# Kernel optimization log

Measured on AMD Instinct MI355X. Metric: run time of the kernel, lower is better.

Reference implementation:

```python
import jax, jax.numpy as jnp
import numpy as np

V = 163842  # ico6 sphere vertex count
C_IN = 64
C_OUT = 64


def setup_inputs() -> dict:
    key = jax.random.key(0)
    k1, k2, k3, k4 = jax.random.split(key, 4)
    x = jax.random.normal(k1, (2, V, C_IN), dtype=jnp.float32)
    neigh_orders = jax.random.randint(k2, (V * 7,), 0, V, dtype=jnp.int64)
    W = jax.random.normal(k3, (C_OUT, 7 * C_IN), dtype=jnp.float32) * 0.05
    b = jax.random.normal(k4, (C_OUT,), dtype=jnp.float32) * 0.05
    return {"x": x, "neigh_orders": neigh_orders, "W": W, "b": b}


def reference(x, neigh_orders, W, b):
    B, Vn, C = x.shape
    # gather 7 neighbors per vertex: (B, V*7, C) -> (B, V, 7*C)
    mat = x[:, neigh_orders].reshape(B, Vn, 7 * C)
    # Linear: mat @ W.T + b -> (B, V, C_out)
    return jnp.einsum('bvk,ok->bvo', mat, W) + b
```

## Files before the change

kernel.cpp:

```cpp
#include <hip/hip_runtime.h>


constexpr int V_ICO   = 163842;
constexpr int M_TOTAL = 2 * V_ICO;
constexpr int X_ELEMS = M_TOTAL * 64;
constexpr int W_ELEMS = 64 * 448;
constexpr int XCH     = X_ELEMS / 8;
constexpr int WCH     = W_ELEMS / 8;

typedef __attribute__((ext_vector_type(4))) float          f32x4;
typedef __attribute__((ext_vector_type(4))) unsigned int   u32x4;
typedef __attribute__((ext_vector_type(8))) unsigned short u16x8;
typedef __attribute__((ext_vector_type(8))) __bf16         bf16x8;

union BF8 { u32x4 q; u16x8 u; bf16x8 v; };

static __device__ __forceinline__ unsigned short f2bf(float f) {
  unsigned int t = __float_as_uint(f);
  t += 0x7FFFu + ((t >> 16) & 1u);
  return (unsigned short)(t >> 16);
}

static __device__ __forceinline__ u32x4 cvt8(f32x4 a, f32x4 b) {
  BF8 r;
  r.u[0] = f2bf(a[0]); r.u[1] = f2bf(a[1]); r.u[2] = f2bf(a[2]); r.u[3] = f2bf(a[3]);
  r.u[4] = f2bf(b[0]); r.u[5] = f2bf(b[1]); r.u[6] = f2bf(b[2]); r.u[7] = f2bf(b[3]);
  return r.q;
}

__global__ __launch_bounds__(256)
void cvt_x_w(const float* __restrict__ x, const float* __restrict__ W,
             u32x4* __restrict__ xbf, u32x4* __restrict__ wbf) {
  const int i = blockIdx.x * blockDim.x + threadIdx.x;
  if (i >= XCH + WCH) return;
  const f32x4* src;
  u32x4* dst;
  if (i < XCH) {
    src = reinterpret_cast<const f32x4*>(x) + 2 * (size_t)i;
    dst = xbf + i;
  } else {
    const int k = i - XCH;
    src = reinterpret_cast<const f32x4*>(W) + 2 * (size_t)k;
    dst = wbf + k;
  }
  f32x4 f0 = src[0], f1 = src[1];
  *dst = cvt8(f0, f1);
}

__global__ __launch_bounds__(256)
void cvt_w_only(const float* __restrict__ W, u32x4* __restrict__ wbf) {
  const int i = blockIdx.x * blockDim.x + threadIdx.x;
  if (i < WCH) {
    const f32x4* src = reinterpret_cast<const f32x4*>(W) + 2 * (size_t)i;
    f32x4 f0 = src[0], f1 = src[1];
    wbf[i] = cvt8(f0, f1);
  }
}

template <int XBF, int WPRE>
__global__ __launch_bounds__(1024, 8)
void gather_mm(const float* __restrict__ x32, const unsigned short* __restrict__ x16,
               const int* __restrict__ neigh,
               const float* __restrict__ W32, const unsigned short* __restrict__ W16,
               const float* __restrict__ bias, float* __restrict__ out) {
  __shared__ __align__(16) unsigned short Wlds[WCH * 8];

  const int tid  = threadIdx.x;
  const int w    = tid >> 6;
  const int lane = tid & 63;
  const int r    = lane & 15;
  const int g    = lane >> 4;
  const int m0   = blockIdx.x * 256 + w * 16;

  int mA = m0 + r;
  if (mA > M_TOTAL - 1) mA = M_TOTAL - 1;
  const int bA = (mA >= V_ICO) ? 1 : 0;
  const int vA = mA - bA * V_ICO;

  int nofs[7];
#pragma unroll
  for (int j = 0; j < 7; ++j) nofs[j] = neigh[vA * 7 + j];

  for (int i = tid; i < WCH; i += 1024) {
    const int kcnt = i >> 6;
    const int l    = i & 63;
    const int row  = ((kcnt & 3) << 4) | (l & 15);
    u32x4 val;
    if constexpr (WPRE) {
      const int c8 = ((kcnt >> 2) << 2) + (l >> 4);
      val = reinterpret_cast<const u32x4*>(W16)[row * 56 + c8];
    } else {
      const int col = ((kcnt >> 2) << 5) + ((l >> 4) << 3);
      const f32x4* p = reinterpret_cast<const f32x4*>(W32 + row * 448 + col);
      val = cvt8(p[0], p[1]);
    }
    *reinterpret_cast<u32x4*>(&Wlds[(size_t)i * 8]) = val;
  }
  __syncthreads();
  if (m0 >= M_TOTAL) return;

  const unsigned short* xb = nullptr;
  const float* xb32 = nullptr;
  if constexpr (XBF) xb   = x16 + (size_t)bA * V_ICO * 64 + (g << 3);
  else               xb32 = x32 + (size_t)bA * V_ICO * 64 + (g << 3);

  const unsigned short* wp = Wlds + (lane << 3);

  const f32x4 zero = {0.f, 0.f, 0.f, 0.f};
  f32x4 acc0 = zero, acc1 = zero, acc2 = zero, acc3 = zero;

#define MFMA_NT(af, nt, kc)                                                 \
    acc##nt = __builtin_amdgcn_mfma_f32_16x16x32_bf16(                      \
        af.v,                                                               \
        *reinterpret_cast<const bf16x8*>(wp + ((kc) * 4 + (nt)) * 512),     \
        acc##nt, 0, 0, 0)

#define COMPUTE_J(dl, dh, j) do {                                           \
    __builtin_amdgcn_s_setprio(1);                                          \
    MFMA_NT(dl, 0, 2*(j));   MFMA_NT(dl, 1, 2*(j));                         \
    MFMA_NT(dl, 2, 2*(j));   MFMA_NT(dl, 3, 2*(j));                         \
    MFMA_NT(dh, 0, 2*(j)+1); MFMA_NT(dh, 1, 2*(j)+1);                       \
    MFMA_NT(dh, 2, 2*(j)+1); MFMA_NT(dh, 3, 2*(j)+1);                       \
    __builtin_amdgcn_s_setprio(0);                                          \
  } while (0)

  if constexpr (XBF) {
#define LOAD_J(dl, dh, j) do {                                              \
      const unsigned short* rp = xb + (size_t)nofs[j] * 64;                 \
      dl.q = *reinterpret_cast<const u32x4*>(rp);                           \
      dh.q = *reinterpret_cast<const u32x4*>(rp + 32);                      \
    } while (0)

    BF8 b0l, b0h, b1l, b1h, b2l, b2h, b3l, b3h;
    LOAD_J(b0l, b0h, 0);
    LOAD_J(b1l, b1h, 1);
    LOAD_J(b2l, b2h, 2);
    LOAD_J(b3l, b3h, 3);
    COMPUTE_J(b0l, b0h, 0); LOAD_J(b0l, b0h, 4);
    COMPUTE_J(b1l, b1h, 1); LOAD_J(b1l, b1h, 5);
    COMPUTE_J(b2l, b2h, 2); LOAD_J(b2l, b2h, 6);
    COMPUTE_J(b3l, b3h, 3);
    COMPUTE_J(b0l, b0h, 4);
    COMPUTE_J(b1l, b1h, 5);
    COMPUTE_J(b2l, b2h, 6);
#undef LOAD_J
  } else {
#pragma unroll
    for (int j = 0; j < 7; ++j) {
      const float* rp = xb32 + (size_t)nofs[j] * 64;
      const f32x4* p0 = reinterpret_cast<const f32x4*>(rp);
      const f32x4* p1 = reinterpret_cast<const f32x4*>(rp + 32);
      BF8 dl, dh;
      dl.q = cvt8(p0[0], p0[1]);
      dh.q = cvt8(p1[0], p1[1]);
      COMPUTE_J(dl, dh, j);
    }
  }
#undef MFMA_NT
#undef COMPUTE_J

  const float bv0 = bias[r], bv1 = bias[16 + r], bv2 = bias[32 + r], bv3 = bias[48 + r];
  const bool full = (m0 + 16 <= M_TOTAL);
#pragma unroll
  for (int q2 = 0; q2 < 4; ++q2) {
    const int mS = m0 + (g << 2) + q2;
    if (full || mS < M_TOTAL) {
      float* o = out + (size_t)mS * 64;
      __builtin_nontemporal_store(acc0[q2] + bv0, o + r);
      __builtin_nontemporal_store(acc1[q2] + bv1, o + 16 + r);
      __builtin_nontemporal_store(acc2[q2] + bv2, o + 32 + r);
      __builtin_nontemporal_store(acc3[q2] + bv3, o + 48 + r);
    }
  }
}

extern "C" void kernel_launch(void* const* d_in, const int* in_sizes, int n_in,
                              void* d_out, int out_size, void* d_ws, size_t ws_size,
                              hipStream_t stream) {
  const float* x    = (const float*)d_in[0];
  const int*   nbr  = (const int*)d_in[1];
  const float* W    = (const float*)d_in[2];
  const float* bias = (const float*)d_in[3];
  float* out = (float*)d_out;

  const size_t xbf_bytes = (size_t)X_ELEMS * 2;
  const size_t wbf_bytes = (size_t)W_ELEMS * 2;
  const int grid_main = (M_TOTAL + 255) / 256;

  if (ws_size >= xbf_bytes + wbf_bytes) {
    u32x4* xbf = (u32x4*)d_ws;
    u32x4* wbf = (u32x4*)((char*)d_ws + xbf_bytes);
    hipLaunchKernelGGL(cvt_x_w, dim3((XCH + WCH + 255) / 256), dim3(256), 0, stream,
                       x, W, xbf, wbf);
    hipLaunchKernelGGL((gather_mm<1, 1>), dim3(grid_main), dim3(1024), 0, stream,
                       x, (const unsigned short*)xbf, nbr,
                       W, (const unsigned short*)wbf, bias, out);
  } else if (ws_size >= wbf_bytes) {
    u32x4* wbf = (u32x4*)d_ws;
    hipLaunchKernelGGL(cvt_w_only, dim3((WCH + 255) / 256), dim3(256), 0, stream, W, wbf);
    hipLaunchKernelGGL((gather_mm<0, 1>), dim3(grid_main), dim3(1024), 0, stream,
                       x, nullptr, nbr, W, (const unsigned short*)wbf, bias, out);
  } else {
    hipLaunchKernelGGL((gather_mm<0, 0>), dim3(grid_main), dim3(1024), 0, stream,
                       x, nullptr, nbr, W, nullptr, bias, out);
  }
}
```

Before: 201.5 us.

## Stage gathered neighbor rows through LDS with async global_load_lds triple buffering

Replaces the register-prefetched gather of bf16 neighbor rows with direct global-to-LDS async loads (global_load_lds) into a per-wave triple buffer, using explicit vmcnt/lgkmcnt waits to overlap gathers with the MFMAs. The goal is to cut VGPR pressure and keep more gathers in flight. It adds 96KB of LDS per block and lowers the launch-bounds occupancy hint, so fewer blocks may fit per CU. The hand-written waitcnt schedule is fragile and depends on how the compiler orders the other memory operations.

New measurement: 202.6 us. No clear change (+0.5%).

```diff
diff --git a/kernel.cpp b/kernel.cpp
--- a/kernel.cpp
+++ b/kernel.cpp
@@ -14,6 +14,11 @@
 typedef __attribute__((ext_vector_type(8))) __bf16         bf16x8;
 
 union BF8 { u32x4 q; u16x8 u; bf16x8 v; };
+
+#define AS1 __attribute__((address_space(1)))
+#define AS3 __attribute__((address_space(3)))
+#define WAITV(N) asm volatile("s_waitcnt vmcnt(" #N ")" ::: "memory")
+#define WAITL0   asm volatile("s_waitcnt lgkmcnt(0)" ::: "memory")
 
 static __device__ __forceinline__ unsigned short f2bf(float f) {
   unsigned int t = __float_as_uint(f);
@@ -58,12 +63,13 @@
 }
 
 template <int XBF, int WPRE>
-__global__ __launch_bounds__(1024, 8)
+__global__ __launch_bounds__(1024, 4)
 void gather_mm(const float* __restrict__ x32, const unsigned short* __restrict__ x16,
                const int* __restrict__ neigh,
                const float* __restrict__ W32, const unsigned short* __restrict__ W16,
                const float* __restrict__ bias, float* __restrict__ out) {
   __shared__ __align__(16) unsigned short Wlds[WCH * 8];
+  __shared__ __align__(16) char gbuf[16 * 3 * 2048];
 
   const int tid  = threadIdx.x;
   const int w    = tid >> 6;
@@ -99,12 +105,8 @@
   __syncthreads();
   if (m0 >= M_TOTAL) return;
 
-  const unsigned short* xb = nullptr;
-  const float* xb32 = nullptr;
-  if constexpr (XBF) xb   = x16 + (size_t)bA * V_ICO * 64 + (g << 3);
-  else               xb32 = x32 + (size_t)bA * V_ICO * 64 + (g << 3);
-
   const unsigned short* wp = Wlds + (lane << 3);
+  char* gs = &gbuf[w * 3 * 2048];
 
   const f32x4 zero = {0.f, 0.f, 0.f, 0.f};
   f32x4 acc0 = zero, acc1 = zero, acc2 = zero, acc3 = zero;
@@ -115,7 +117,7 @@
         *reinterpret_cast<const bf16x8*>(wp + ((kc) * 4 + (nt)) * 512),     \
         acc##nt, 0, 0, 0)
 
-#define COMPUTE_J(dl, dh, j) do {                                           \
+#define MFMA_8(dl, dh, j) do {                                              \
     __builtin_amdgcn_s_setprio(1);                                          \
     MFMA_NT(dl, 0, 2*(j));   MFMA_NT(dl, 1, 2*(j));                         \
     MFMA_NT(dl, 2, 2*(j));   MFMA_NT(dl, 3, 2*(j));                         \
@@ -125,26 +127,36 @@
   } while (0)
 
   if constexpr (XBF) {
-#define LOAD_J(dl, dh, j) do {                                              \
-      const unsigned short* rp = xb + (size_t)nofs[j] * 64;                 \
-      dl.q = *reinterpret_cast<const u32x4*>(rp);                           \
-      dh.q = *reinterpret_cast<const u32x4*>(rp + 32);                      \
+    const unsigned short* xb = x16 + (size_t)bA * V_ICO * 64 + (g << 3);
+
+#define ISSUE_J(so, j) do {                                                  \
+      const unsigned short* rp_ = xb + (size_t)nofs[j] * 64;                 \
+      __builtin_amdgcn_global_load_lds((const AS1 unsigned int*)rp_,         \
+          (AS3 unsigned int*)(gs + (so)), 16, 0, 0);                         \
+      __builtin_amdgcn_global_load_lds((const AS1 unsigned int*)(rp_ + 32),  \
+          (AS3 unsigned int*)(gs + (so) + 1024), 16, 0, 0);                  \
     } while (0)
 
-    BF8 b0l, b0h, b1l, b1h, b2l, b2h, b3l, b3h;
-    LOAD_J(b0l, b0h, 0);
-    LOAD_J(b1l, b1h, 1);
-    LOAD_J(b2l, b2h, 2);
-    LOAD_J(b3l, b3h, 3);
-    COMPUTE_J(b0l, b0h, 0); LOAD_J(b0l, b0h, 4);
-    COMPUTE_J(b1l, b1h, 1); LOAD_J(b1l, b1h, 5);
-    COMPUTE_J(b2l, b2h, 2); LOAD_J(b2l, b2h, 6);
-    COMPUTE_J(b3l, b3h, 3);
-    COMPUTE_J(b0l, b0h, 4);
-    COMPUTE_J(b1l, b1h, 5);
-    COMPUTE_J(b2l, b2h, 6);
-#undef LOAD_J
+#define COMP_J(so, j) do {                                                   \
+      BF8 dl, dh;                                                            \
+      dl.q = *reinterpret_cast<const u32x4*>(gs + (so) + (lane << 4));       \
+      dh.q = *reinterpret_cast<const u32x4*>(gs + (so) + 1024 + (lane << 4));\
+      MFMA_8(dl, dh, j);                                                     \
+    } while (0)
+
+    WAITV(0);
+    ISSUE_J(0, 0); ISSUE_J(2048, 1); ISSUE_J(4096, 2);
+    WAITV(4); COMP_J(0, 0);    WAITL0; ISSUE_J(0, 3);
+    WAITV(4); COMP_J(2048, 1); WAITL0; ISSUE_J(2048, 4);
+    WAITV(4); COMP_J(4096, 2); WAITL0; ISSUE_J(4096, 5);
+    WAITV(4); COMP_J(0, 3);    WAITL0; ISSUE_J(0, 6);
+    WAITV(4); COMP_J(2048, 4);
+    WAITV(2); COMP_J(4096, 5);
+    WAITV(0); COMP_J(0, 6);
+#undef ISSUE_J
+#undef COMP_J
   } else {
+    const float* xb32 = x32 + (size_t)bA * V_ICO * 64 + (g << 3);
 #pragma unroll
     for (int j = 0; j < 7; ++j) {
       const float* rp = xb32 + (size_t)nofs[j] * 64;
@@ -153,11 +165,11 @@
       BF8 dl, dh;
       dl.q = cvt8(p0[0], p0[1]);
       dh.q = cvt8(p1[0], p1[1]);
-      COMPUTE_J(dl, dh, j);
+      MFMA_8(dl, dh, j);
     }
   }
 #undef MFMA_NT
-#undef COMPUTE_J
+#undef MFMA_8
 
   const float bv0 = bias[r], bv1 = bias[16 + r], bv2 = bias[32 + r], bv3 = bias[48 + r];
   const bool full = (m0 + 16 <= M_TOTAL);
```

## Process both batches per vertex, bounce epilogue through LDS, prefetch bf16 x

Applied to the files above, without the earlier changes.

Each wave now handles 16 vertices for both batch elements. The neighbor indices and each W fragment read from LDS serve two MFMA chains, and the grid is halved. Output tiles are staged through a padded LDS buffer so each lane writes a contiguous float4 instead of scattered scalar stores. A separate warm-up kernel streams the converted bf16 x array beforehand to pull it into the last-level cache. In exchange, per-block LDS use grows to roughly 125 KB, which caps occupancy, and the warm-up pass adds a full read of x.

Measured after the change: 208.4 us. +3.4%, slower.

```diff
diff --git a/kernel.cpp b/kernel.cpp
--- a/kernel.cpp
+++ b/kernel.cpp
@@ -7,6 +7,7 @@
 constexpr int W_ELEMS = 64 * 448;
 constexpr int XCH     = X_ELEMS / 8;
 constexpr int WCH     = W_ELEMS / 8;
+constexpr int GRID_MM = (V_ICO + 255) / 256;
 
 typedef __attribute__((ext_vector_type(4))) float          f32x4;
 typedef __attribute__((ext_vector_type(4))) unsigned int   u32x4;
@@ -57,25 +58,35 @@
   }
 }
 
+__global__ __launch_bounds__(256)
+void warm_l3(const u32x4* __restrict__ p, int nchunks) {
+  unsigned int a0 = 0, a1 = 0, a2 = 0, a3 = 0;
+  const int stride = gridDim.x * blockDim.x;
+  for (int i = blockIdx.x * blockDim.x + threadIdx.x; i < nchunks; i += stride) {
+    u32x4 v = p[i];
+    a0 ^= v[0]; a1 ^= v[1]; a2 ^= v[2]; a3 ^= v[3];
+  }
+  asm volatile("" :: "v"(a0), "v"(a1), "v"(a2), "v"(a3));
+}
+
 template <int XBF, int WPRE>
-__global__ __launch_bounds__(1024, 8)
+__global__ __launch_bounds__(1024, 4)
 void gather_mm(const float* __restrict__ x32, const unsigned short* __restrict__ x16,
                const int* __restrict__ neigh,
                const float* __restrict__ W32, const unsigned short* __restrict__ W16,
                const float* __restrict__ bias, float* __restrict__ out) {
   __shared__ __align__(16) unsigned short Wlds[WCH * 8];
+  __shared__ __align__(16) float Bounce[16][16][68];
 
   const int tid  = threadIdx.x;
   const int w    = tid >> 6;
   const int lane = tid & 63;
   const int r    = lane & 15;
   const int g    = lane >> 4;
-  const int m0   = blockIdx.x * 256 + w * 16;
-
-  int mA = m0 + r;
-  if (mA > M_TOTAL - 1) mA = M_TOTAL - 1;
-  const int bA = (mA >= V_ICO) ? 1 : 0;
-  const int vA = mA - bA * V_ICO;
+  const int v0   = blockIdx.x * 256 + w * 16;
+
+  int vA = v0 + r;
+  if (vA > V_ICO - 1) vA = V_ICO - 1;
 
   int nofs[7];
 #pragma unroll
@@ -97,81 +108,119 @@
     *reinterpret_cast<u32x4*>(&Wlds[(size_t)i * 8]) = val;
   }
   __syncthreads();
-  if (m0 >= M_TOTAL) return;
-
-  const unsigned short* xb = nullptr;
-  const float* xb32 = nullptr;
-  if constexpr (XBF) xb   = x16 + (size_t)bA * V_ICO * 64 + (g << 3);
-  else               xb32 = x32 + (size_t)bA * V_ICO * 64 + (g << 3);
+  if (v0 >= V_ICO) return;
 
   const unsigned short* wp = Wlds + (lane << 3);
 
   const f32x4 zero = {0.f, 0.f, 0.f, 0.f};
-  f32x4 acc0 = zero, acc1 = zero, acc2 = zero, acc3 = zero;
-
-#define MFMA_NT(af, nt, kc)                                                 \
-    acc##nt = __builtin_amdgcn_mfma_f32_16x16x32_bf16(                      \
-        af.v,                                                               \
-        *reinterpret_cast<const bf16x8*>(wp + ((kc) * 4 + (nt)) * 512),     \
-        acc##nt, 0, 0, 0)
-
-#define COMPUTE_J(dl, dh, j) do {                                           \
-    __builtin_amdgcn_s_setprio(1);                                          \
-    MFMA_NT(dl, 0, 2*(j));   MFMA_NT(dl, 1, 2*(j));                         \
-    MFMA_NT(dl, 2, 2*(j));   MFMA_NT(dl, 3, 2*(j));                         \
-    MFMA_NT(dh, 0, 2*(j)+1); MFMA_NT(dh, 1, 2*(j)+1);                       \
-    MFMA_NT(dh, 2, 2*(j)+1); MFMA_NT(dh, 3, 2*(j)+1);                       \
-    __builtin_amdgcn_s_setprio(0);                                          \
+  f32x4 aA0 = zero, aA1 = zero, aA2 = zero, aA3 = zero;
+  f32x4 aB0 = zero, aB1 = zero, aB2 = zero, aB3 = zero;
+
+#define FR(kc, nt) (*reinterpret_cast<const bf16x8*>(wp + ((kc) * 4 + (nt)) * 512))
+
+#define COMPJ(s0, s1, s2, s3, j) do {                                        \
+    __builtin_amdgcn_s_setprio(1);                                           \
+    bf16x8 f_;                                                               \
+    f_ = FR(2*(j), 0);                                                       \
+    aA0 = __builtin_amdgcn_mfma_f32_16x16x32_bf16(s0.v, f_, aA0, 0, 0, 0);   \
+    aB0 = __builtin_amdgcn_mfma_f32_16x16x32_bf16(s2.v, f_, aB0, 0, 0, 0);   \
+    f_ = FR(2*(j), 1);                                                       \
+    aA1 = __builtin_amdgcn_mfma_f32_16x16x32_bf16(s0.v, f_, aA1, 0, 0, 0);   \
+    aB1 = __builtin_amdgcn_mfma_f32_16x16x32_bf16(s2.v, f_, aB1, 0, 0, 0);   \
+    f_ = FR(2*(j), 2);                                                       \
+    aA2 = __builtin_amdgcn_mfma_f32_16x16x32_bf16(s0.v, f_, aA2, 0, 0, 0);   \
+    aB2 = __builtin_amdgcn_mfma_f32_16x16x32_bf16(s2.v, f_, aB2, 0, 0, 0);   \
+    f_ = FR(2*(j), 3);                                                       \
+    aA3 = __builtin_amdgcn_mfma_f32_16x16x32_bf16(s0.v, f_, aA3, 0, 0, 0);   \
+    aB3 = __builtin_amdgcn_mfma_f32_16x16x32_bf16(s2.v, f_, aB3, 0, 0, 0);   \
+    f_ = FR(2*(j)+1, 0);                                                     \
+    aA0 = __builtin_amdgcn_mfma_f32_16x16x32_bf16(s1.v, f_, aA0, 0, 0, 0);   \
+    aB0 = __builtin_amdgcn_mfma_f32_16x16x32_bf16(s3.v, f_, aB0, 0, 0, 0);   \
+    f_ = FR(2*(j)+1, 1);                                                     \
+    aA1 = __builtin_amdgcn_mfma_f32_16x16x32_bf16(s1.v, f_, aA1, 0, 0, 0);   \
+    aB1 = __builtin_amdgcn_mfma_f32_16x16x32_bf16(s3.v, f_, aB1, 0, 0, 0);   \
+    f_ = FR(2*(j)+1, 2);                                                     \
+    aA2 = __builtin_amdgcn_mfma_f32_16x16x32_bf16(s1.v, f_, aA2, 0, 0, 0);   \
+    aB2 = __builtin_amdgcn_mfma_f32_16x16x32_bf16(s3.v, f_, aB2, 0, 0, 0);   \
+    f_ = FR(2*(j)+1, 3);                                                     \
+    aA3 = __builtin_amdgcn_mfma_f32_16x16x32_bf16(s1.v, f_, aA3, 0, 0, 0);   \
+    aB3 = __builtin_amdgcn_mfma_f32_16x16x32_bf16(s3.v, f_, aB3, 0, 0, 0);   \
+    __builtin_amdgcn_s_setprio(0);                                           \
   } while (0)
 
   if constexpr (XBF) {
-#define LOAD_J(dl, dh, j) do {                                              \
-      const unsigned short* rp = xb + (size_t)nofs[j] * 64;                 \
-      dl.q = *reinterpret_cast<const u32x4*>(rp);                           \
-      dh.q = *reinterpret_cast<const u32x4*>(rp + 32);                      \
+    const unsigned short* xb0 = x16 + (g << 3);
+    const unsigned short* xb1 = xb0 + (size_t)V_ICO * 64;
+
+#define LOADJ(s0, s1, s2, s3, j) do {                                        \
+      const size_t ro = (size_t)nofs[j] * 64;                                \
+      s0.q = *reinterpret_cast<const u32x4*>(xb0 + ro);                      \
+      s1.q = *reinterpret_cast<const u32x4*>(xb0 + ro + 32);                 \
+      s2.q = *reinterpret_cast<const u32x4*>(xb1 + ro);                      \
+      s3.q = *reinterpret_cast<const u32x4*>(xb1 + ro + 32);                 \
     } while (0)
 
-    BF8 b0l, b0h, b1l, b1h, b2l, b2h, b3l, b3h;
-    LOAD_J(b0l, b0h, 0);
-    LOAD_J(b1l, b1h, 1);
-    LOAD_J(b2l, b2h, 2);
-    LOAD_J(b3l, b3h, 3);
-    COMPUTE_J(b0l, b0h, 0); LOAD_J(b0l, b0h, 4);
-    COMPUTE_J(b1l, b1h, 1); LOAD_J(b1l, b1h, 5);
-    COMPUTE_J(b2l, b2h, 2); LOAD_J(b2l, b2h, 6);
-    COMPUTE_J(b3l, b3h, 3);
-    COMPUTE_J(b0l, b0h, 4);
-    COMPUTE_J(b1l, b1h, 5);
-    COMPUTE_J(b2l, b2h, 6);
-#undef LOAD_J
+    BF8 pA0, pA1, pA2, pA3, pB0, pB1, pB2, pB3;
+    LOADJ(pA0, pA1, pA2, pA3, 0);
+    LOADJ(pB0, pB1, pB2, pB3, 1);
+    COMPJ(pA0, pA1, pA2, pA3, 0); LOADJ(pA0, pA1, pA2, pA3, 2);
+    COMPJ(pB0, pB1, pB2, pB3, 1); LOADJ(pB0, pB1, pB2, pB3, 3);
+    COMPJ(pA0, pA1, pA2, pA3, 2); LOADJ(pA0, pA1, pA2, pA3, 4);
+    COMPJ(pB0, pB1, pB2, pB3, 3); LOADJ(pB0, pB1, pB2, pB3, 5);
+    COMPJ(pA0, pA1, pA2, pA3, 4); LOADJ(pA0, pA1, pA2, pA3, 6);
+    COMPJ(pB0, pB1, pB2, pB3, 5);
+    COMPJ(pA0, pA1, pA2, pA3, 6);
+#undef LOADJ
   } else {
+    const float* xb0 = x32 + (g << 3);
+    const float* xb1 = xb0 + (size_t)V_ICO * 64;
 #pragma unroll
     for (int j = 0; j < 7; ++j) {
-      const float* rp = xb32 + (size_t)nofs[j] * 64;
-      const f32x4* p0 = reinterpret_cast<const f32x4*>(rp);
-      const f32x4* p1 = reinterpret_cast<const f32x4*>(rp + 32);
-      BF8 dl, dh;
-      dl.q = cvt8(p0[0], p0[1]);
-      dh.q = cvt8(p1[0], p1[1]);
-      COMPUTE_J(dl, dh, j);
-    }
-  }
-#undef MFMA_NT
-#undef COMPUTE_J
-
-  const float bv0 = bias[r], bv1 = bias[16 + r], bv2 = bias[32 + r], bv3 = bias[48 + r];
-  const bool full = (m0 + 16 <= M_TOTAL);
-#pragma unroll
-  for (int q2 = 0; q2 < 4; ++q2) {
-    const int mS = m0 + (g << 2) + q2;
-    if (full || mS < M_TOTAL) {
-      float* o = out + (size_t)mS * 64;
-      __builtin_nontemporal_store(acc0[q2] + bv0, o + r);
-      __builtin_nontemporal_store(acc1[q2] + bv1, o + 16 + r);
-      __builtin_nontemporal_store(acc2[q2] + bv2, o + 32 + r);
-      __builtin_nontemporal_store(acc3[q2] + bv3, o + 48 + r);
-    }
-  }
+      const size_t ro = (size_t)nofs[j] * 64;
+      BF8 s0, s1, s2, s3;
+      const f32x4* p = reinterpret_cast<const f32x4*>(xb0 + ro);
+      s0.q = cvt8(p[0], p[1]);
+      p = reinterpret_cast<const f32x4*>(xb0 + ro + 32);
+      s1.q = cvt8(p[0], p[1]);
+      p = reinterpret_cast<const f32x4*>(xb1 + ro);
+      s2.q = cvt8(p[0], p[1]);
+      p = reinterpret_cast<const f32x4*>(xb1 + ro + 32);
+      s3.q = cvt8(p[0], p[1]);
+      COMPJ(s0, s1, s2, s3, j);
+    }
+  }
+#undef COMPJ
+#undef FR
+
+  float* bw = &Bounce[w][0][0];
+  const f32x4 biasf = *reinterpret_cast<const f32x4*>(bias + (r << 2));
+  const bool full = (v0 + 16 <= V_ICO);
+
+  auto epilogue = [&](const f32x4& A0, const f32x4& A1, const f32x4& A2,
+                      const f32x4& A3, size_t rowbase) {
+#pragma unroll
+    for (int q2 = 0; q2 < 4; ++q2) {
+      bw[(g * 4 + q2) * 68 +  0 + r] = A0[q2];
+      bw[(g * 4 + q2) * 68 + 16 + r] = A1[q2];
+      bw[(g * 4 + q2) * 68 + 32 + r] = A2[q2];
+      bw[(g * 4 + q2) * 68 + 48 + r] = A3[q2];
+    }
+    asm volatile("s_waitcnt lgkmcnt(0)" ::: "memory");
+#pragma unroll
+    for (int q2 = 0; q2 < 4; ++q2) {
+      const int rowIt = g * 4 + q2;
+      f32x4 v = *reinterpret_cast<const f32x4*>(&bw[rowIt * 68 + (r << 2)]);
+      v = v + biasf;
+      if (full || v0 + rowIt < V_ICO) {
+        __builtin_nontemporal_store(
+            v, reinterpret_cast<f32x4*>(out + (rowbase + rowIt) * 64 + (r << 2)));
+      }
+    }
+    asm volatile("s_waitcnt lgkmcnt(0)" ::: "memory");
+  };
+
+  epilogue(aA0, aA1, aA2, aA3, (size_t)v0);
+  epilogue(aB0, aB1, aB2, aB3, (size_t)V_ICO + v0);
 }
 
 extern "C" void kernel_launch(void* const* d_in, const int* in_sizes, int n_in,
@@ -185,23 +234,24 @@
 
   const size_t xbf_bytes = (size_t)X_ELEMS * 2;
   const size_t wbf_bytes = (size_t)W_ELEMS * 2;
-  const int grid_main = (M_TOTAL + 255) / 256;
 
   if (ws_size >= xbf_bytes + wbf_bytes) {
     u32x4* xbf = (u32x4*)d_ws;
     u32x4* wbf = (u32x4*)((char*)d_ws + xbf_bytes);
     hipLaunchKernelGGL(cvt_x_w, dim3((XCH + WCH + 255) / 256), dim3(256), 0, stream,
                        x, W, xbf, wbf);
-    hipLaunchKernelGGL((gather_mm<1, 1>), dim3(grid_main), dim3(1024), 0, stream,
+    hipLaunchKernelGGL(warm_l3, dim3(2048), dim3(256), 0, stream,
+                       (const u32x4*)xbf, XCH);
+    hipLaunchKernelGGL((gather_mm<1, 1>), dim3(GRID_MM), dim3(1024), 0, stream,
                        x, (const unsigned short*)xbf, nbr,
                        W, (const unsigned short*)wbf, bias, out);
   } else if (ws_size >= wbf_bytes) {
     u32x4* wbf = (u32x4*)d_ws;
     hipLaunchKernelGGL(cvt_w_only, dim3((WCH + 255) / 256), dim3(256), 0, stream, W, wbf);
-    hipLaunchKernelGGL((gather_mm<0, 1>), dim3(grid_main), dim3(1024), 0, stream,
+    hipLaunchKernelGGL((gather_mm<0, 1>), dim3(GRID_MM), dim3(1024), 0, stream,
                        x, nullptr, nbr, W, (const unsigned short*)wbf, bias, out);
   } else {
-    hipLaunchKernelGGL((gather_mm<0, 0>), dim3(grid_main), dim3(1024), 0, stream,
+    hipLaunchKernelGGL((gather_mm<0, 0>), dim3(GRID_MM), dim3(1024), 0, stream,
                        x, nullptr, nbr, W, nullptr, bias, out);
   }
 }
```
